# Optimization experiments

Hardware: AMD Instinct MI355X
Metric: run time of the kernel (lower is better)

Reference implementation:

```python
import jax, jax.numpy as jnp
import numpy as np
import math

WINDOW_SIZE = 11
SIGMA = 1.5

def _gaussian_window(window_size, channel):
    g = np.array([math.exp(-(x - window_size // 2) ** 2 / (2 * SIGMA ** 2)) for x in range(window_size)], dtype=np.float32)
    g = g / g.sum()
    w2d = np.outer(g, g).astype(np.float32)  # [K,K]
    # depthwise kernel, OIHW with O=channel, I=1
    return jnp.asarray(np.broadcast_to(w2d, (channel, 1, window_size, window_size)).copy())

def _dwconv(x, window):
    # x: [B,C,H,W], window: [C,1,K,K]; 'same' padding depthwise conv
    pad = WINDOW_SIZE // 2
    return jax.lax.conv_general_dilated(
        x, window, window_strides=(1, 1), padding=[(pad, pad), (pad, pad)],
        feature_group_count=x.shape[1],
        dimension_numbers=('NCHW', 'OIHW', 'NCHW'))

def setup_inputs() -> dict:
    key = jax.random.key(0)
    k1, k2 = jax.random.split(key)
    pred = jax.random.uniform(k1, (16, 3, 512, 512), dtype=jnp.float32)
    label = jax.random.uniform(k2, (16, 3, 512, 512), dtype=jnp.float32)
    return {"pred": pred, "label": label}

def reference(pred, label):
    img1, img2 = pred, label
    channel = img1.shape[1]
    window = _gaussian_window(WINDOW_SIZE, channel)
    mu1 = _dwconv(img1, window)
    mu2 = _dwconv(img2, window)
    mu1_sq = mu1 * mu1
    mu2_sq = mu2 * mu2
    mu1_mu2 = mu1 * mu2
    sigma1_sq = _dwconv(img1 * img1, window) - mu1_sq
    sigma2_sq = _dwconv(img2 * img2, window) - mu2_sq
    sigma12 = _dwconv(img1 * img2, window) - mu1_mu2
    C1, C2 = 0.01 ** 2, 0.03 ** 2
    ssim_map = ((2 * mu1_mu2 + C1) * (2 * sigma12 + C2)) / ((mu1_sq + mu2_sq + C1) * (sigma1_sq + sigma2_sq + C2))
    return 1.0 - ssim_map.mean()
```

## Files before the change

kernel.cpp:

```cpp
#include <hip/hip_runtime.h>

#define IMG_W 512
#define IMG_H 512
#define NPLANES 48
#define NPIX 12582912.0
#define HT_STRIDE 44
#define NBLOCKS (16*16*48)

__global__ __launch_bounds__(256) void ssim_fused_kernel(
    const float* __restrict__ pred,
    const float* __restrict__ label,
    float* __restrict__ partial)
{
    __shared__ float hT[5][32][HT_STRIDE];

    const int tid = threadIdx.x;
    const int ox = blockIdx.x * 32;
    const int oy = blockIdx.y * 32;
    const int plane = blockIdx.z;
    const float* __restrict__ xp = pred  + (size_t)plane * IMG_W * IMG_H;
    const float* __restrict__ yp = label + (size_t)plane * IMG_W * IMG_H;

    float w[11];
    {
        float s = 0.f;
        #pragma unroll
        for (int i = 0; i < 11; ++i) {
            float d = (float)(i - 5);
            w[i] = expf(-d * d / 4.5f);
            s += w[i];
        }
        float inv = 1.0f / s;
        #pragma unroll
        for (int i = 0; i < 11; ++i) w[i] *= inv;
    }

    const bool xInterior = (blockIdx.x != 0) && (blockIdx.x != (IMG_W / 32 - 1));
    for (int i = tid; i < 336; i += 256) {
        int r  = i >> 3;
        int g  = i & 7;
        int gy = oy - 5 + r;
        int c0 = ox + g * 4;

        float bx_[24], by_[24];
        bool rowok = ((unsigned)gy < (unsigned)IMG_H);
        if (!rowok) {
            #pragma unroll
            for (int j = 0; j < 24; ++j) { bx_[j] = 0.f; by_[j] = 0.f; }
        } else if (xInterior) {
            const float4* px4 = reinterpret_cast<const float4*>(xp + gy * IMG_W + (c0 - 8));
            const float4* py4 = reinterpret_cast<const float4*>(yp + gy * IMG_W + (c0 - 8));
            #pragma unroll
            for (int j = 0; j < 6; ++j) {
                float4 a = px4[j];
                float4 b = py4[j];
                bx_[4*j+0] = a.x; bx_[4*j+1] = a.y; bx_[4*j+2] = a.z; bx_[4*j+3] = a.w;
                by_[4*j+0] = b.x; by_[4*j+1] = b.y; by_[4*j+2] = b.z; by_[4*j+3] = b.w;
            }
        } else {
            #pragma unroll
            for (int j = 0; j < 24; ++j) {
                int col = c0 - 8 + j;
                bool ok = ((unsigned)col < (unsigned)IMG_W);
                bx_[j] = ok ? xp[gy * IMG_W + col] : 0.f;
                by_[j] = ok ? yp[gy * IMG_W + col] : 0.f;
            }
        }

        float a0[4] = {0,0,0,0}, a1[4] = {0,0,0,0}, a2[4] = {0,0,0,0},
              a3[4] = {0,0,0,0}, a4[4] = {0,0,0,0};
        #pragma unroll
        for (int j = 3; j <= 16; ++j) {
            float xv = bx_[j], yv = by_[j];
            float xx = xv * xv, yy = yv * yv, xy = xv * yv;
            #pragma unroll
            for (int o = 0; o < 4; ++o) {
                int k = j - 3 - o;
                if (k >= 0 && k <= 10) {
                    float wk = w[k];
                    a0[o] += wk * xv;
                    a1[o] += wk * yv;
                    a2[o] += wk * xx;
                    a3[o] += wk * yy;
                    a4[o] += wk * xy;
                }
            }
        }
        #pragma unroll
        for (int o = 0; o < 4; ++o) {
            int c = g * 4 + o;
            hT[0][c][r] = a0[o];
            hT[1][c][r] = a1[o];
            hT[2][c][r] = a2[o];
            hT[3][c][r] = a3[o];
            hT[4][c][r] = a4[o];
        }
    }
    __syncthreads();

    {
        int c  = tid & 31;
        int rg = tid >> 5;
        int rb = rg * 4;

        float m[5][4];
        #pragma unroll
        for (int f = 0; f < 5; ++f) {
            const float4* p = reinterpret_cast<const float4*>(&hT[f][c][rb]);
            float4 v0 = p[0], v1 = p[1], v2 = p[2], v3 = p[3];
            float vv[16] = { v0.x, v0.y, v0.z, v0.w,
                             v1.x, v1.y, v1.z, v1.w,
                             v2.x, v2.y, v2.z, v2.w,
                             v3.x, v3.y, v3.z, v3.w };
            #pragma unroll
            for (int o = 0; o < 4; ++o) {
                float s = 0.f;
                #pragma unroll
                for (int k = 0; k < 11; ++k) s += w[k] * vv[o + k];
                m[f][o] = s;
            }
        }

        float lsum = 0.f;
        #pragma unroll
        for (int o = 0; o < 4; ++o) {
            float mu1 = m[0][o], mu2 = m[1][o];
            float mu1s = mu1 * mu1, mu2s = mu2 * mu2, mu12 = mu1 * mu2;
            float s1  = m[2][o] - mu1s;
            float s2  = m[3][o] - mu2s;
            float s12 = m[4][o] - mu12;
            const float C1 = 1e-4f, C2 = 9e-4f;
            float num = (2.f * mu12 + C1) * (2.f * s12 + C2);
            float den = (mu1s + mu2s + C1) * (s1 + s2 + C2);
            lsum += num / den;
        }

        #pragma unroll
        for (int off = 32; off > 0; off >>= 1)
            lsum += __shfl_down(lsum, off, 64);

        __shared__ float wsum[4];
        if ((tid & 63) == 0) wsum[tid >> 6] = lsum;
        __syncthreads();
        if (tid == 0) {
            int bid = (blockIdx.z * gridDim.y + blockIdx.y) * gridDim.x + blockIdx.x;
            partial[bid] = wsum[0] + wsum[1] + wsum[2] + wsum[3];
        }
    }
}

__global__ __launch_bounds__(256) void ssim_finalize_kernel(
    const float* __restrict__ partial, float* __restrict__ out)
{
    double s = 0.0;
    for (int i = threadIdx.x; i < NBLOCKS; i += 256) s += (double)partial[i];
    #pragma unroll
    for (int off = 32; off > 0; off >>= 1) s += __shfl_down(s, off, 64);
    __shared__ double ws[4];
    if ((threadIdx.x & 63) == 0) ws[threadIdx.x >> 6] = s;
    __syncthreads();
    if (threadIdx.x == 0)
        out[0] = 1.0f - (float)((ws[0] + ws[1] + ws[2] + ws[3]) / NPIX);
}

extern "C" void kernel_launch(void* const* d_in, const int* in_sizes, int n_in,
                              void* d_out, int out_size, void* d_ws, size_t ws_size,
                              hipStream_t stream) {
    const float* pred  = (const float*)d_in[0];
    const float* label = (const float*)d_in[1];
    float* out = (float*)d_out;
    float* partial = (float*)d_ws;

    dim3 grid(IMG_W / 32, IMG_H / 32, NPLANES);
    ssim_fused_kernel<<<grid, 256, 0, stream>>>(pred, label, partial);
    ssim_finalize_kernel<<<1, 256, 0, stream>>>(partial, out);
}
```

Measured before the change: 192.8 us.

## Replace shared-memory tiles with per-thread column streaming and register ring buffer

The tiled kernel, which staged horizontal convolution results in LDS, is replaced by a streaming design. Each thread owns one column of a 64-row strip. It computes the horizontal 11-tap sums for each row from global memory and keeps the last 11 rows of five statistics in a register ring buffer for the vertical pass. This removes LDS traffic and the block barrier, and uses a fast reciprocal for the division. The cost is that each thread does 11 scalar loads per row, relying on cache for neighbour reuse, and the grid shrinks to 768 blocks, which may leave the GPU underoccupied. The ring buffer is indexed with a modulo, which may force it into scratch memory if the loop does not fully unroll.

New measurement: 279.3 us. +44.8%, slower.

```diff
diff --git a/kernel.cpp b/kernel.cpp
--- a/kernel.cpp
+++ b/kernel.cpp
@@ -4,22 +4,21 @@
 #define IMG_H 512
 #define NPLANES 48
 #define NPIX 12582912.0
-#define HT_STRIDE 44
-#define NBLOCKS (16*16*48)
+#define NBLOCKS 768
 
-__global__ __launch_bounds__(256) void ssim_fused_kernel(
+__global__ __launch_bounds__(256) void ssim_stream_kernel(
     const float* __restrict__ pred,
     const float* __restrict__ label,
     float* __restrict__ partial)
 {
-    __shared__ float hT[5][32][HT_STRIDE];
-
-    const int tid = threadIdx.x;
-    const int ox = blockIdx.x * 32;
-    const int oy = blockIdx.y * 32;
+    const int tid   = threadIdx.x;
+    const int cg    = blockIdx.x;
+    const int col   = cg * 64 + (tid & 63);
+    const int strip = blockIdx.y * 4 + (tid >> 6);
+    const int oy    = strip * 64;
     const int plane = blockIdx.z;
-    const float* __restrict__ xp = pred  + (size_t)plane * IMG_W * IMG_H;
-    const float* __restrict__ yp = label + (size_t)plane * IMG_W * IMG_H;
+    const float* __restrict__ xp = pred  + (size_t)plane * (IMG_W * IMG_H);
+    const float* __restrict__ yp = label + (size_t)plane * (IMG_W * IMG_H);
 
     float w[11];
     {
@@ -35,117 +34,97 @@
         for (int i = 0; i < 11; ++i) w[i] *= inv;
     }
 
-    const bool xInterior = (blockIdx.x != 0) && (blockIdx.x != (IMG_W / 32 - 1));
-    for (int i = tid; i < 336; i += 256) {
-        int r  = i >> 3;
-        int g  = i & 7;
-        int gy = oy - 5 + r;
-        int c0 = ox + g * 4;
+    const bool edge = (cg == 0) || (cg == 7);
+    const int  c0   = col - 5;
+    int   cc[11];
+    float mf[11];
+    #pragma unroll
+    for (int j = 0; j < 11; ++j) {
+        int c = c0 + j;
+        cc[j] = min(max(c, 0), IMG_W - 1);
+        mf[j] = ((unsigned)c < (unsigned)IMG_W) ? 1.0f : 0.0f;
+    }
 
-        float bx_[24], by_[24];
-        bool rowok = ((unsigned)gy < (unsigned)IMG_H);
-        if (!rowok) {
-            #pragma unroll
-            for (int j = 0; j < 24; ++j) { bx_[j] = 0.f; by_[j] = 0.f; }
-        } else if (xInterior) {
-            const float4* px4 = reinterpret_cast<const float4*>(xp + gy * IMG_W + (c0 - 8));
-            const float4* py4 = reinterpret_cast<const float4*>(yp + gy * IMG_W + (c0 - 8));
-            #pragma unroll
-            for (int j = 0; j < 6; ++j) {
-                float4 a = px4[j];
-                float4 b = py4[j];
-                bx_[4*j+0] = a.x; bx_[4*j+1] = a.y; bx_[4*j+2] = a.z; bx_[4*j+3] = a.w;
-                by_[4*j+0] = b.x; by_[4*j+1] = b.y; by_[4*j+2] = b.z; by_[4*j+3] = b.w;
-            }
-        } else {
-            #pragma unroll
-            for (int j = 0; j < 24; ++j) {
-                int col = c0 - 8 + j;
-                bool ok = ((unsigned)col < (unsigned)IMG_W);
-                bx_[j] = ok ? xp[gy * IMG_W + col] : 0.f;
-                by_[j] = ok ? yp[gy * IMG_W + col] : 0.f;
-            }
-        }
+    float ring[5][11];
+    float lsum = 0.f;
 
-        float a0[4] = {0,0,0,0}, a1[4] = {0,0,0,0}, a2[4] = {0,0,0,0},
-              a3[4] = {0,0,0,0}, a4[4] = {0,0,0,0};
+    for (int rr = 0; rr < 7; ++rr) {
         #pragma unroll
-        for (int j = 3; j <= 16; ++j) {
-            float xv = bx_[j], yv = by_[j];
-            float xx = xv * xv, yy = yv * yv, xy = xv * yv;
-            #pragma unroll
-            for (int o = 0; o < 4; ++o) {
-                int k = j - 3 - o;
-                if (k >= 0 && k <= 10) {
-                    float wk = w[k];
-                    a0[o] += wk * xv;
-                    a1[o] += wk * yv;
-                    a2[o] += wk * xx;
-                    a3[o] += wk * yy;
-                    a4[o] += wk * xy;
+        for (int p = 0; p < 11; ++p) {
+            const int r = rr * 11 + p;
+            if (r < 74) {
+                const int gr = oy - 5 + r;
+                float hx = 0.f, hy = 0.f, hxx = 0.f, hyy = 0.f, hxy = 0.f;
+                if ((unsigned)gr < (unsigned)IMG_H) {
+                    const float* __restrict__ xr = xp + gr * IMG_W;
+                    const float* __restrict__ yr = yp + gr * IMG_W;
+                    if (edge) {
+                        #pragma unroll
+                        for (int j = 0; j < 11; ++j) {
+                            float xv = xr[cc[j]] * mf[j];
+                            float yv = yr[cc[j]] * mf[j];
+                            float wj = w[j];
+                            hx  += wj * xv;
+                            hy  += wj * yv;
+                            hxx += wj * xv * xv;
+                            hyy += wj * yv * yv;
+                            hxy += wj * xv * yv;
+                        }
+                    } else {
+                        #pragma unroll
+                        for (int j = 0; j < 11; ++j) {
+                            float xv = xr[c0 + j];
+                            float yv = yr[c0 + j];
+                            float wj = w[j];
+                            hx  += wj * xv;
+                            hy  += wj * yv;
+                            hxx += wj * xv * xv;
+                            hyy += wj * yv * yv;
+                            hxy += wj * xv * yv;
+                        }
+                    }
+                }
+                ring[0][p] = hx;
+                ring[1][p] = hy;
+                ring[2][p] = hxx;
+                ring[3][p] = hyy;
+                ring[4][p] = hxy;
+
+                if (r >= 10) {
+                    float mu1 = 0.f, mu2 = 0.f, cxx = 0.f, cyy = 0.f, cxy = 0.f;
+                    #pragma unroll
+                    for (int k = 0; k < 11; ++k) {
+                        const int kk = (p + 1 + k) % 11;
+                        float wk = w[k];
+                        mu1 += wk * ring[0][kk];
+                        mu2 += wk * ring[1][kk];
+                        cxx += wk * ring[2][kk];
+                        cyy += wk * ring[3][kk];
+                        cxy += wk * ring[4][kk];
+                    }
+                    float mu1s = mu1 * mu1, mu2s = mu2 * mu2, mu12 = mu1 * mu2;
+                    float s1  = cxx - mu1s;
+                    float s2  = cyy - mu2s;
+                    float s12 = cxy - mu12;
+                    const float C1 = 1e-4f, C2 = 9e-4f;
+                    float num = (2.f * mu12 + C1) * (2.f * s12 + C2);
+                    float den = (mu1s + mu2s + C1) * (s1 + s2 + C2);
+                    lsum += num * __builtin_amdgcn_rcpf(den);
                 }
             }
         }
-        #pragma unroll
-        for (int o = 0; o < 4; ++o) {
-            int c = g * 4 + o;
-            hT[0][c][r] = a0[o];
-            hT[1][c][r] = a1[o];
-            hT[2][c][r] = a2[o];
-            hT[3][c][r] = a3[o];
-            hT[4][c][r] = a4[o];
-        }
     }
+
+    #pragma unroll
+    for (int off = 32; off > 0; off >>= 1)
+        lsum += __shfl_down(lsum, off, 64);
+
+    __shared__ float wsum[4];
+    if ((tid & 63) == 0) wsum[tid >> 6] = lsum;
     __syncthreads();
-
-    {
-        int c  = tid & 31;
-        int rg = tid >> 5;
-        int rb = rg * 4;
-
-        float m[5][4];
-        #pragma unroll
-        for (int f = 0; f < 5; ++f) {
-            const float4* p = reinterpret_cast<const float4*>(&hT[f][c][rb]);
-            float4 v0 = p[0], v1 = p[1], v2 = p[2], v3 = p[3];
-            float vv[16] = { v0.x, v0.y, v0.z, v0.w,
-                             v1.x, v1.y, v1.z, v1.w,
-                             v2.x, v2.y, v2.z, v2.w,
-                             v3.x, v3.y, v3.z, v3.w };
-            #pragma unroll
-            for (int o = 0; o < 4; ++o) {
-                float s = 0.f;
-                #pragma unroll
-                for (int k = 0; k < 11; ++k) s += w[k] * vv[o + k];
-                m[f][o] = s;
-            }
-        }
-
-        float lsum = 0.f;
-        #pragma unroll
-        for (int o = 0; o < 4; ++o) {
-            float mu1 = m[0][o], mu2 = m[1][o];
-            float mu1s = mu1 * mu1, mu2s = mu2 * mu2, mu12 = mu1 * mu2;
-            float s1  = m[2][o] - mu1s;
-            float s2  = m[3][o] - mu2s;
-            float s12 = m[4][o] - mu12;
-            const float C1 = 1e-4f, C2 = 9e-4f;
-            float num = (2.f * mu12 + C1) * (2.f * s12 + C2);
-            float den = (mu1s + mu2s + C1) * (s1 + s2 + C2);
-            lsum += num / den;
-        }
-
-        #pragma unroll
-        for (int off = 32; off > 0; off >>= 1)
-            lsum += __shfl_down(lsum, off, 64);
-
-        __shared__ float wsum[4];
-        if ((tid & 63) == 0) wsum[tid >> 6] = lsum;
-        __syncthreads();
-        if (tid == 0) {
-            int bid = (blockIdx.z * gridDim.y + blockIdx.y) * gridDim.x + blockIdx.x;
-            partial[bid] = wsum[0] + wsum[1] + wsum[2] + wsum[3];
-        }
+    if (tid == 0) {
+        int bid = (blockIdx.z * 2 + blockIdx.y) * 8 + blockIdx.x;
+        partial[bid] = wsum[0] + wsum[1] + wsum[2] + wsum[3];
     }
 }
 
@@ -171,7 +150,7 @@
     float* out = (float*)d_out;
     float* partial = (float*)d_ws;
 
-    dim3 grid(IMG_W / 32, IMG_H / 32, NPLANES);
-    ssim_fused_kernel<<<grid, 256, 0, stream>>>(pred, label, partial);
+    dim3 grid(8, 2, NPLANES);
+    ssim_stream_kernel<<<grid, 256, 0, stream>>>(pred, label, partial);
     ssim_finalize_kernel<<<1, 256, 0, stream>>>(partial, out);
 }
```

## Swizzle shared transpose buffer, hardcode Gaussian weights, use fast reciprocal

Applied to the files above, without the earlier changes.

Replaces the padded shared-memory transpose layout with a stride-64 XOR-swizzled layout, so the horizontal-pass writes and the vertical-pass float4 reads hit fewer LDS bank conflicts. It also hardcodes the Gaussian weights as constants instead of computing expf per thread, and replaces the division with a hardware reciprocal. The finalize kernel is widened to 1024 threads. The reciprocal is approximate, and the larger stride raises shared memory per block from about 28KB to 40KB, which may reduce occupancy.

Result: slower. 213.5 us (+10.7%).

```diff
diff --git a/kernel.cpp b/kernel.cpp
--- a/kernel.cpp
+++ b/kernel.cpp
@@ -4,36 +4,28 @@
 #define IMG_H 512
 #define NPLANES 48
 #define NPIX 12582912.0
-#define HT_STRIDE 44
+#define ST 64
+#define FSZ (32 * ST)
 #define NBLOCKS (16*16*48)
+
 
 __global__ __launch_bounds__(256) void ssim_fused_kernel(
     const float* __restrict__ pred,
     const float* __restrict__ label,
     float* __restrict__ partial)
 {
-    __shared__ float hT[5][32][HT_STRIDE];
+    __shared__ float hT[5 * FSZ];
+
+    const float w[11] = { 0.00102838f, 0.00759876f, 0.03600077f, 0.10936069f,
+                          0.21300554f, 0.26601173f, 0.21300554f, 0.10936069f,
+                          0.03600077f, 0.00759876f, 0.00102838f };
 
     const int tid = threadIdx.x;
     const int ox = blockIdx.x * 32;
     const int oy = blockIdx.y * 32;
     const int plane = blockIdx.z;
-    const float* __restrict__ xp = pred  + (size_t)plane * IMG_W * IMG_H;
-    const float* __restrict__ yp = label + (size_t)plane * IMG_W * IMG_H;
-
-    float w[11];
-    {
-        float s = 0.f;
-        #pragma unroll
-        for (int i = 0; i < 11; ++i) {
-            float d = (float)(i - 5);
-            w[i] = expf(-d * d / 4.5f);
-            s += w[i];
-        }
-        float inv = 1.0f / s;
-        #pragma unroll
-        for (int i = 0; i < 11; ++i) w[i] *= inv;
-    }
+    const float* __restrict__ xp = pred  + (size_t)plane * (IMG_W * IMG_H);
+    const float* __restrict__ yp = label + (size_t)plane * (IMG_W * IMG_H);
 
     const bool xInterior = (blockIdx.x != 0) && (blockIdx.x != (IMG_W / 32 - 1));
     for (int i = tid; i < 336; i += 256) {
@@ -86,28 +78,38 @@
                 }
             }
         }
+
+        int wb = g * (4 * ST) + ((((r >> 2) ^ g) << 2) | (r & 3));
         #pragma unroll
         for (int o = 0; o < 4; ++o) {
-            int c = g * 4 + o;
-            hT[0][c][r] = a0[o];
-            hT[1][c][r] = a1[o];
-            hT[2][c][r] = a2[o];
-            hT[3][c][r] = a3[o];
-            hT[4][c][r] = a4[o];
+            hT[wb + o*ST + 0*FSZ] = a0[o];
+            hT[wb + o*ST + 1*FSZ] = a1[o];
+            hT[wb + o*ST + 2*FSZ] = a2[o];
+            hT[wb + o*ST + 3*FSZ] = a3[o];
+            hT[wb + o*ST + 4*FSZ] = a4[o];
         }
     }
     __syncthreads();
 
+    float lsum = 0.f;
     {
         int c  = tid & 31;
         int rg = tid >> 5;
-        int rb = rg * 4;
+        int sc = c >> 2;
+        int cb = c * ST;
+
+        int d0 = cb + 4 * ((rg + 0) ^ sc);
+        int d1 = cb + 4 * ((rg + 1) ^ sc);
+        int d2 = cb + 4 * ((rg + 2) ^ sc);
+        int d3 = cb + 4 * ((rg + 3) ^ sc);
 
         float m[5][4];
         #pragma unroll
         for (int f = 0; f < 5; ++f) {
-            const float4* p = reinterpret_cast<const float4*>(&hT[f][c][rb]);
-            float4 v0 = p[0], v1 = p[1], v2 = p[2], v3 = p[3];
+            float4 v0 = *reinterpret_cast<const float4*>(&hT[f*FSZ + d0]);
+            float4 v1 = *reinterpret_cast<const float4*>(&hT[f*FSZ + d1]);
+            float4 v2 = *reinterpret_cast<const float4*>(&hT[f*FSZ + d2]);
+            float4 v3 = *reinterpret_cast<const float4*>(&hT[f*FSZ + d3]);
             float vv[16] = { v0.x, v0.y, v0.z, v0.w,
                              v1.x, v1.y, v1.z, v1.w,
                              v2.x, v2.y, v2.z, v2.w,
@@ -121,7 +123,6 @@
             }
         }
 
-        float lsum = 0.f;
         #pragma unroll
         for (int o = 0; o < 4; ++o) {
             float mu1 = m[0][o], mu2 = m[1][o];
@@ -132,35 +133,39 @@
             const float C1 = 1e-4f, C2 = 9e-4f;
             float num = (2.f * mu12 + C1) * (2.f * s12 + C2);
             float den = (mu1s + mu2s + C1) * (s1 + s2 + C2);
-            lsum += num / den;
+            lsum += num * __builtin_amdgcn_rcpf(den);
         }
+    }
 
-        #pragma unroll
-        for (int off = 32; off > 0; off >>= 1)
-            lsum += __shfl_down(lsum, off, 64);
+    #pragma unroll
+    for (int off = 32; off > 0; off >>= 1)
+        lsum += __shfl_down(lsum, off, 64);
 
-        __shared__ float wsum[4];
-        if ((tid & 63) == 0) wsum[tid >> 6] = lsum;
-        __syncthreads();
-        if (tid == 0) {
-            int bid = (blockIdx.z * gridDim.y + blockIdx.y) * gridDim.x + blockIdx.x;
-            partial[bid] = wsum[0] + wsum[1] + wsum[2] + wsum[3];
-        }
+    __shared__ float wsum[4];
+    if ((tid & 63) == 0) wsum[tid >> 6] = lsum;
+    __syncthreads();
+    if (tid == 0) {
+        int bid = (blockIdx.z * gridDim.y + blockIdx.y) * gridDim.x + blockIdx.x;
+        partial[bid] = wsum[0] + wsum[1] + wsum[2] + wsum[3];
     }
 }
 
-__global__ __launch_bounds__(256) void ssim_finalize_kernel(
+__global__ __launch_bounds__(1024) void ssim_finalize_kernel(
     const float* __restrict__ partial, float* __restrict__ out)
 {
     double s = 0.0;
-    for (int i = threadIdx.x; i < NBLOCKS; i += 256) s += (double)partial[i];
+    for (int i = threadIdx.x; i < NBLOCKS; i += 1024) s += (double)partial[i];
     #pragma unroll
     for (int off = 32; off > 0; off >>= 1) s += __shfl_down(s, off, 64);
-    __shared__ double ws[4];
+    __shared__ double ws[16];
     if ((threadIdx.x & 63) == 0) ws[threadIdx.x >> 6] = s;
     __syncthreads();
-    if (threadIdx.x == 0)
-        out[0] = 1.0f - (float)((ws[0] + ws[1] + ws[2] + ws[3]) / NPIX);
+    if (threadIdx.x == 0) {
+        double t = 0.0;
+        #pragma unroll
+        for (int k = 0; k < 16; ++k) t += ws[k];
+        out[0] = 1.0f - (float)(t / NPIX);
+    }
 }
 
 extern "C" void kernel_launch(void* const* d_in, const int* in_sizes, int n_in,
@@ -173,5 +178,5 @@
 
     dim3 grid(IMG_W / 32, IMG_H / 32, NPLANES);
     ssim_fused_kernel<<<grid, 256, 0, stream>>>(pred, label, partial);
-    ssim_finalize_kernel<<<1, 256, 0, stream>>>(partial, out);
+    ssim_finalize_kernel<<<1, 1024, 0, stream>>>(partial, out);
 }
```
